# Kernel tuning notes

Hardware: AMD Instinct MI355X
Metric: run time of the kernel (lower is better)

Reference implementation:

```python
import jax, jax.numpy as jnp
import numpy as np


def spmm(src, dst, w, x, n):
    # out[i] = sum_{e: dst[e]==i} w[e] * x[src[e]]  == th.spmm(adj, x) with adj COO (dst=row, src=col)
    return jax.ops.segment_sum(x[src] * w[:, None], dst, num_segments=n)


def gcn(x, ei, w, W1, b1, W2, b2):
    # GCN.forward: relu(gc1(x, adj)) -> dropout(eval: identity) -> gc2(x, adj)
    n = x.shape[0]
    src, dst = ei[1], ei[0]
    h = jax.nn.relu(spmm(src, dst, w, x @ W1, n) + b1)
    return spmm(src, dst, w, h @ W2, n) + b2


def setup_inputs() -> dict:
    key = jax.random.key(0)
    ks = jax.random.split(key, 24)
    Nd, Ns = 100000, 50000
    Fd, Fs, H1, H2 = 256, 256, 256, 128
    DEG = 32
    Ed, Es = Nd * DEG, Ns * DEG
    inp = {}
    inp['drug_sim_feat'] = jax.random.normal(ks[0], (Nd, Fd), jnp.float32)
    inp['drug_edge_index'] = jax.random.randint(ks[1], (2, Ed), 0, Nd, jnp.int32)
    inp['drug_edge_weight'] = jax.random.uniform(ks[2], (Ed,), jnp.float32) / DEG
    inp['drug_feat_edge_index'] = jax.random.randint(ks[3], (2, Ed), 0, Nd, jnp.int32)
    inp['drug_feat_edge_weight'] = jax.random.uniform(ks[4], (Ed,), jnp.float32) / DEG
    inp['disease_sim_feat'] = jax.random.normal(ks[5], (Ns, Fs), jnp.float32)
    inp['dis_edge_index'] = jax.random.randint(ks[6], (2, Es), 0, Ns, jnp.int32)
    inp['dis_edge_weight'] = jax.random.uniform(ks[7], (Es,), jnp.float32) / DEG
    inp['dis_feat_edge_index'] = jax.random.randint(ks[8], (2, Es), 0, Ns, jnp.int32)
    inp['dis_feat_edge_weight'] = jax.random.uniform(ks[9], (Es,), jnp.float32) / DEG
    # params: uniform(-stdv, stdv), stdv = 1/sqrt(out_features) as in reset_parameters
    def unif(k, shape, out_f):
        s = 1.0 / np.sqrt(out_f)
        return jax.random.uniform(k, shape, jnp.float32, -s, s)
    inp['W1d'] = unif(ks[10], (Fd, H1), H1); inp['b1d'] = unif(ks[11], (H1,), H1)
    inp['W2d'] = unif(ks[12], (H1, H2), H2); inp['b2d'] = unif(ks[13], (H2,), H2)
    inp['W1s'] = unif(ks[14], (Fs, H1), H1); inp['b1s'] = unif(ks[15], (H1,), H1)
    inp['W2s'] = unif(ks[16], (H1, H2), H2); inp['b2s'] = unif(ks[17], (H2,), H2)
    # fusion Linears (nhid2*2 -> nhid2); kaiming-ish uniform
    fs = 1.0 / np.sqrt(2 * H2)
    inp['Wfd'] = jax.random.uniform(ks[18], (2 * H2, H2), jnp.float32, -fs, fs)
    inp['bfd'] = jax.random.uniform(ks[19], (H2,), jnp.float32, -fs, fs)
    inp['Wfs'] = jax.random.uniform(ks[20], (2 * H2, H2), jnp.float32, -fs, fs)
    inp['bfs'] = jax.random.uniform(ks[21], (H2,), jnp.float32, -fs, fs)
    return inp


def reference(drug_sim_feat, drug_edge_index, drug_edge_weight,
              drug_feat_edge_index, drug_feat_edge_weight,
              disease_sim_feat, dis_edge_index, dis_edge_weight,
              dis_feat_edge_index, dis_feat_edge_weight,
              W1d, b1d, W2d, b2d, W1s, b1s, W2s, b2s,
              Wfd, bfd, Wfs, bfs):
    # dropout in eval mode (identity)
    emb1_sim = gcn(drug_sim_feat, drug_edge_index, drug_edge_weight, W1d, b1d, W2d, b2d)
    emb2_sim = gcn(disease_sim_feat, dis_edge_index, dis_edge_weight, W1s, b1s, W2s, b2s)
    emb1_feat = gcn(drug_sim_feat, drug_feat_edge_index, drug_feat_edge_weight, W1d, b1d, W2d, b2d)
    emb2_feat = gcn(disease_sim_feat, dis_feat_edge_index, dis_feat_edge_weight, W1s, b1s, W2s, b2s)
    emb1 = jax.nn.relu(jnp.concatenate([emb1_sim, emb1_feat], axis=1) @ Wfd + bfd)
    emb2 = jax.nn.relu(jnp.concatenate([emb2_sim, emb2_feat], axis=1) @ Wfs + bfs)
    return (emb1, emb2, emb1_sim, emb1_feat, emb2_sim, emb2_feat)
```

## Files before the change

kernel.cpp:

```cpp
#include <hip/hip_runtime.h>

typedef _Float16 f16;
typedef __attribute__((ext_vector_type(8))) _Float16 f16x8;
typedef __attribute__((ext_vector_type(4))) float f32x4;

__device__ inline ushort f2h_bits(float f) {
    f16 h = (f16)f;
    return __builtin_bit_cast(ushort, h);
}

struct T6 {
    const float* s[6];
    ushort* d[6];
    int N[6];
};

__global__ __launch_bounds__(256) void transpose6_k(T6 a) {
    __shared__ ushort tile[32][33];
    const int z = blockIdx.z;
    const int K = 256, N = a.N[z];
    int k0 = blockIdx.x * 32, n0 = blockIdx.y * 32;
    if (n0 >= N) return;
    const float* W = a.s[z];
    ushort* Wt = a.d[z];
    int tx = threadIdx.x & 31, ty = threadIdx.x >> 5;
    #pragma unroll
    for (int i = 0; i < 32; i += 8)
        tile[ty + i][tx] = f2h_bits(W[(size_t)(k0 + ty + i) * N + n0 + tx]);
    __syncthreads();
    #pragma unroll
    for (int i = 0; i < 32; i += 8)
        Wt[(size_t)(n0 + ty + i) * K + k0 + tx] = tile[tx][ty + i];
}

struct GraphDesc {
    const int* ei;
    const float* w;
    int E, n, NB, bstoff;
    int* row_ptr;
    int2* perm;
};
struct G4 { GraphDesc g[4]; };

__global__ __launch_bounds__(256) void hist_b(G4 a, int* __restrict__ bcounts) {
    const GraphDesc& G = a.g[blockIdx.y];
    const int e0 = blockIdx.x * 4096;
    if (e0 >= G.E) return;
    __shared__ int h[512];
    int t = threadIdx.x;
    h[t] = 0; h[t + 256] = 0;
    __syncthreads();
    #pragma unroll
    for (int k = 0; k < 16; ++k) {
        int i = e0 + t + k * 256;
        if (i < G.E) atomicAdd(&h[((uint)G.ei[i]) >> 8], 1);
    }
    __syncthreads();
    int* bc = bcounts + blockIdx.y * 512;
    for (int b = t; b < 512; b += 256)
        if (h[b]) atomicAdd(&bc[b], h[b]);
}

__global__ __launch_bounds__(256) void scan_b(G4 a, const int* __restrict__ bcounts,
                                              int* __restrict__ bbase, int* __restrict__ bcursor) {
    const int gidx = blockIdx.x;
    const GraphDesc& G = a.g[gidx];
    const int* bc = bcounts + gidx * 512;
    int* base = bbase + gidx * 513;
    int* cur  = bcursor + gidx * 512;
    int t = threadIdx.x, lane = t & 63, wave = t >> 6;
    int v0 = bc[2 * t], v1 = bc[2 * t + 1];
    int s = v0 + v1;
    int incl = s;
    for (int off = 1; off < 64; off <<= 1) {
        int u = __shfl_up(incl, off);
        if (lane >= off) incl += u;
    }
    __shared__ int wsum[4];
    if (lane == 63) wsum[wave] = incl;
    __syncthreads();
    int excl = incl - s;
    for (int wv = 0; wv < wave; ++wv) excl += wsum[wv];
    base[2 * t] = excl;      cur[2 * t] = excl;
    base[2 * t + 1] = excl + v0; cur[2 * t + 1] = excl + v0;
    if (t == 0) { base[512] = G.E; G.row_ptr[G.n] = G.E; }
}

__global__ __launch_bounds__(256) void scatter_b(G4 a, int* __restrict__ bcursor,
                                                 int2* __restrict__ bst) {
    const GraphDesc& G = a.g[blockIdx.y];
    const int e0 = blockIdx.x * 4096;
    if (e0 >= G.E) return;
    __shared__ int hist[512], excl[512], sbase[512], lcur[512];
    __shared__ int2 stage[4096];
    __shared__ ushort sbin[4096];
    const int t = threadIdx.x, lane = t & 63, wave = t >> 6;
    const int cnt = min(4096, G.E - e0);
    int* bcur = bcursor + blockIdx.y * 512;

    hist[t] = 0; hist[t + 256] = 0;
    __syncthreads();

    int   d[16], s[16];
    float wv[16];
    #pragma unroll
    for (int k = 0; k < 16; ++k) {
        int i = t + k * 256;
        if (i < cnt) {
            d[k]  = G.ei[e0 + i];
            s[k]  = G.ei[(size_t)G.E + e0 + i];
            wv[k] = G.w[e0 + i];
            atomicAdd(&hist[((uint)d[k]) >> 8], 1);
        }
    }
    __syncthreads();

    {
        int v0 = hist[2 * t], v1 = hist[2 * t + 1];
        int sum = v0 + v1;
        int incl = sum;
        for (int off = 1; off < 64; off <<= 1) {
            int u = __shfl_up(incl, off);
            if (lane >= off) incl += u;
        }
        __shared__ int wsum[4];
        if (lane == 63) wsum[wave] = incl;
        __syncthreads();
        int e = incl - sum;
        for (int wvv = 0; wvv < wave; ++wvv) e += wsum[wvv];
        excl[2 * t] = e; excl[2 * t + 1] = e + v0;
    }
    __syncthreads();

    for (int b = t; b < 512; b += 256) {
        int c = hist[b];
        sbase[b] = c ? atomicAdd(&bcur[b], c) : 0;
        lcur[b] = excl[b];
    }
    __syncthreads();

    #pragma unroll
    for (int k = 0; k < 16; ++k) {
        int i = t + k * 256;
        if (i < cnt) {
            int bin = ((uint)d[k]) >> 8;
            int pos = atomicAdd(&lcur[bin], 1);
            stage[pos] = make_int2((s[k] << 8) | (d[k] & 255), __float_as_int(wv[k]));
            sbin[pos] = (ushort)bin;
        }
    }
    __syncthreads();

    #pragma unroll
    for (int k = 0; k < 16; ++k) {
        int i = t + k * 256;
        if (i < cnt) {
            int2 r = stage[i];
            int bin = sbin[i];
            bst[(size_t)G.bstoff + sbase[bin] + i - excl[bin]] = r;
        }
    }
}

__global__ __launch_bounds__(256) void finalize_b(G4 a, const int* __restrict__ bbase,
                                                  const int2* __restrict__ bst) {
    const GraphDesc& G = a.g[blockIdx.y];
    const int b = blockIdx.x;
    if (b >= G.NB) return;
    __shared__ int hist[256], cur[256], wsum[4];
    const int t = threadIdx.x, lane = t & 63, wave = t >> 6;
    const int* base = bbase + blockIdx.y * 513;
    const int lo = base[b], hi = base[b + 1];
    const int2* bg = bst + G.bstoff;
    hist[t] = 0;
    __syncthreads();
    for (int i = lo + t; i < hi; i += 256)
        atomicAdd(&hist[bg[i].x & 255], 1);
    __syncthreads();
    int v = hist[t];
    int incl = v;
    for (int off = 1; off < 64; off <<= 1) {
        int u = __shfl_up(incl, off);
        if (lane >= off) incl += u;
    }
    if (lane == 63) wsum[wave] = incl;
    __syncthreads();
    int excl = incl - v;
    for (int wv = 0; wv < wave; ++wv) excl += wsum[wv];
    const int r0 = b << 8;
    const int nrows = min(256, G.n - r0);
    if (t < nrows) G.row_ptr[r0 + t] = lo + excl;
    cur[t] = lo + excl;
    __syncthreads();
    for (int i = lo + t; i < hi; i += 256) {
        int2 r = bg[i];
        int local = r.x & 255;
        int slot = atomicAdd(&cur[local], 1);
        G.perm[slot] = make_int2(r.x >> 8, r.y);
    }
}

struct PairDesc {
    const int2* perm[2];
    const int*  rp[2];
    ushort*     outh[2];
};

template<int C>
__global__ __launch_bounds__(256) void spmm_pair_f16(
    const f16* __restrict__ x, PairDesc a, const float* __restrict__ bias, int n)
{
    const int g = blockIdx.y;
    const int wave = threadIdx.x >> 6, lane = threadIdx.x & 63;
    const int row = blockIdx.x * 4 + wave;
    if (row >= n) return;
    const int2* __restrict__ perm = a.perm[g];
    const int*  __restrict__ rp   = a.rp[g];
    const int F = 64 * C;
    const int e0 = rp[row], e1 = rp[row + 1];
    float acc[C] = {};
    const int laneoff = lane * C;

    for (int eb = e0; eb < e1; eb += 64) {
        int idx = eb + lane;
        int myS = 0; int myW = 0;
        if (idx < e1) { int2 rec = perm[idx]; myS = rec.x; myW = rec.y; }
        int m = min(64, e1 - eb);
        for (int j0 = 0; j0 < m; j0 += 8) {
            #pragma unroll
            for (int u = 0; u < 8; ++u) {
                int j = j0 + u;
                int   s = __builtin_amdgcn_readlane(myS, j);
                float w = __int_as_float(__builtin_amdgcn_readlane(myW, j));
                const f16* xr = x + (size_t)((uint)s * (uint)F) + laneoff;
                union { uint2 u2; f16 h[4]; } cv;
                cv.u2 = *reinterpret_cast<const uint2*>(xr);
                acc[0] = fmaf((float)cv.h[0], w, acc[0]);
                acc[1] = fmaf((float)cv.h[1], w, acc[1]);
                acc[2] = fmaf((float)cv.h[2], w, acc[2]);
                acc[3] = fmaf((float)cv.h[3], w, acc[3]);
            }
        }
    }

    #pragma unroll
    for (int c = 0; c < C; ++c) {
        float v = acc[c] + bias[laneoff + c];
        acc[c] = fmaxf(v, 0.f);
    }
    *reinterpret_cast<ushort4*>(a.outh[g] + (size_t)row * F + laneoff) =
        make_ushort4(f2h_bits(acc[0]), f2h_bits(acc[1]), f2h_bits(acc[2]), f2h_bits(acc[3]));
}

__global__ __launch_bounds__(256) void spmm_l2_f16(
    const f16* __restrict__ x,
    const int2* __restrict__ perm,
    const int* __restrict__ row_ptr, const float* __restrict__ bias,
    ushort* __restrict__ out_h, float* __restrict__ out_f, int n)
{
    const int wave = threadIdx.x >> 6, lane = threadIdx.x & 63;
    const int row = blockIdx.x * 4 + wave;
    if (row >= n) return;
    const int F = 128;
    const int e0 = row_ptr[row], e1 = row_ptr[row + 1];
    float acc[2] = {};
    const int laneoff = lane * 2;

    for (int eb = e0; eb < e1; eb += 64) {
        int idx = eb + lane;
        int myS = 0; int myW = 0;
        if (idx < e1) { int2 rec = perm[idx]; myS = rec.x; myW = rec.y; }
        int m = min(64, e1 - eb);
        for (int j0 = 0; j0 < m; j0 += 8) {
            #pragma unroll
            for (int u = 0; u < 8; ++u) {
                int j = j0 + u;
                int   s = __builtin_amdgcn_readlane(myS, j);
                float w = __int_as_float(__builtin_amdgcn_readlane(myW, j));
                union { uint u1; f16 h[2]; } cv;
                cv.u1 = *reinterpret_cast<const uint*>(x + (size_t)((uint)s * (uint)F) + laneoff);
                acc[0] = fmaf((float)cv.h[0], w, acc[0]);
                acc[1] = fmaf((float)cv.h[1], w, acc[1]);
            }
        }
    }

    acc[0] += bias[laneoff];
    acc[1] += bias[laneoff + 1];
    size_t ob = (size_t)row * F + laneoff;
    *reinterpret_cast<float2*>(out_f + ob) = make_float2(acc[0], acc[1]);
    *reinterpret_cast<ushort2*>(out_h + ob) = make_ushort2(f2h_bits(acc[0]), f2h_bits(acc[1]));
}

template<bool SWAP, bool CVTA, bool FUSE, bool RELU, bool BIAS, bool F32OUT>
__global__ __launch_bounds__(256) void gemm_mfma(
    const void* __restrict__ Av, const ushort* __restrict__ A2,
    const ushort* __restrict__ Bt, const float* __restrict__ bias,
    ushort* __restrict__ Ch, float* __restrict__ Cf,
    int M, int N, int K)
{
    __shared__ ushort Asb[128 * 32];
    __shared__ ushort Bsb[128 * 32];
    const int tid = threadIdx.x;
    const int lane = tid & 63, wave = tid >> 6;
    const int wr = wave >> 1, wc = wave & 1;
    const int bm = (SWAP ? blockIdx.y : blockIdx.x) * 128;
    const int bn = (SWAP ? blockIdx.x : blockIdx.y) * 128;

    f32x4 acc[4][4] = {};

    for (int k0 = 0; k0 < K; k0 += 32) {
        #pragma unroll
        for (int h = 0; h < 2; ++h) {
            int slot = tid + 256 * h;
            int r = slot >> 2, cb = slot & 3;
            int row = bm + r;
            uint4 v = make_uint4(0, 0, 0, 0);
            if (row < M) {
                int kk = k0 + cb * 8;
                if (CVTA) {
                    const float* Af = (const float*)Av;
                    float4 lo = *reinterpret_cast<const float4*>(Af + (size_t)row * K + kk);
                    float4 hi = *reinterpret_cast<const float4*>(Af + (size_t)row * K + kk + 4);
                    ushort h8[8] = { f2h_bits(lo.x), f2h_bits(lo.y), f2h_bits(lo.z), f2h_bits(lo.w),
                                     f2h_bits(hi.x), f2h_bits(hi.y), f2h_bits(hi.z), f2h_bits(hi.w) };
                    v = *reinterpret_cast<const uint4*>(h8);
                } else if (FUSE) {
                    const ushort* Ap = (kk < 128) ? (const ushort*)Av : A2;
                    v = *reinterpret_cast<const uint4*>(Ap + (size_t)row * 128 + (kk & 127));
                } else {
                    v = *reinterpret_cast<const uint4*>((const ushort*)Av + (size_t)row * K + kk);
                }
            }
            int scb = cb ^ ((r >> 1) & 3);
            *reinterpret_cast<uint4*>(&Asb[r * 32 + scb * 8]) = v;
        }
        #pragma unroll
        for (int h = 0; h < 2; ++h) {
            int slot = tid + 256 * h;
            int r = slot >> 2, cb = slot & 3;
            uint4 v = *reinterpret_cast<const uint4*>(Bt + (size_t)(bn + r) * K + k0 + cb * 8);
            int scb = cb ^ ((r >> 1) & 3);
            *reinterpret_cast<uint4*>(&Bsb[r * 32 + scb * 8]) = v;
        }
        __syncthreads();

        f16x8 fa[4], fb[4];
        #pragma unroll
        for (int i = 0; i < 4; ++i) {
            int r = wr * 64 + i * 16 + (lane & 15);
            int scb = (lane >> 4) ^ ((r >> 1) & 3);
            fa[i] = *reinterpret_cast<const f16x8*>(&Asb[r * 32 + scb * 8]);
        }
        #pragma unroll
        for (int j = 0; j < 4; ++j) {
            int r = wc * 64 + j * 16 + (lane & 15);
            int scb = (lane >> 4) ^ ((r >> 1) & 3);
            fb[j] = *reinterpret_cast<const f16x8*>(&Bsb[r * 32 + scb * 8]);
        }
        #pragma unroll
        for (int i = 0; i < 4; ++i)
            #pragma unroll
            for (int j = 0; j < 4; ++j)
                acc[i][j] = __builtin_amdgcn_mfma_f32_16x16x32_f16(fa[i], fb[j], acc[i][j], 0, 0, 0);
        __syncthreads();
    }

    #pragma unroll
    for (int i = 0; i < 4; ++i) {
        #pragma unroll
        for (int r4 = 0; r4 < 4; ++r4) {
            int row = bm + wr * 64 + i * 16 + (lane >> 4) * 4 + r4;
            if (row >= M) continue;
            #pragma unroll
            for (int j = 0; j < 4; ++j) {
                int col = bn + wc * 64 + j * 16 + (lane & 15);
                float v = acc[i][j][r4];
                if (BIAS) v += bias[col];
                if (RELU) v = fmaxf(v, 0.f);
                if (F32OUT) Cf[(size_t)row * N + col] = v;
                else        Ch[(size_t)row * N + col] = f2h_bits(v);
            }
        }
    }
}

extern "C" void kernel_launch(void* const* d_in, const int* in_sizes, int n_in,
                              void* d_out, int out_size, void* d_ws, size_t ws_size,
                              hipStream_t stream) {
    const float* Xd       = (const float*)d_in[0];
    const int*   eid_sim  = (const int*)  d_in[1];
    const float* wd_sim   = (const float*)d_in[2];
    const int*   eid_feat = (const int*)  d_in[3];
    const float* wd_feat  = (const float*)d_in[4];
    const float* Xs       = (const float*)d_in[5];
    const int*   eis_sim  = (const int*)  d_in[6];
    const float* ws_sim   = (const float*)d_in[7];
    const int*   eis_feat = (const int*)  d_in[8];
    const float* ws_feat  = (const float*)d_in[9];
    const float* W1d = (const float*)d_in[10]; const float* b1d = (const float*)d_in[11];
    const float* W2d = (const float*)d_in[12]; const float* b2d = (const float*)d_in[13];
    const float* W1s = (const float*)d_in[14]; const float* b1s = (const float*)d_in[15];
    const float* W2s = (const float*)d_in[16]; const float* b2s = (const float*)d_in[17];
    const float* Wfd = (const float*)d_in[18]; const float* bfd = (const float*)d_in[19];
    const float* Wfs = (const float*)d_in[20]; const float* bfs = (const float*)d_in[21];

    const int Fd = 256, H1 = 256, H2 = 128;
    const int Nd = in_sizes[0] / Fd;
    const int Ns = in_sizes[5] / Fd;
    const int Ed = in_sizes[2];
    const int Es = in_sizes[7];

    float* out    = (float*)d_out;
    float* o_emb1 = out;
    float* o_emb2 = o_emb1 + (size_t)Nd * H2;
    float* o_e1s  = o_emb2 + (size_t)Ns * H2;
    float* o_e1f  = o_e1s  + (size_t)Nd * H2;
    float* o_e2s  = o_e1f  + (size_t)Nd * H2;
    float* o_e2f  = o_e2s  + (size_t)Ns * H2;

    char* p = (char*)d_ws;
    auto alloc = [&](size_t bytes) { char* q = p; p += (bytes + 255) & ~(size_t)255; return q; };
    ushort* xw1   = (ushort*)alloc((size_t)Nd * 256 * 2);
    ushort* hbuf0 = (ushort*)alloc((size_t)Nd * 256 * 2);
    ushort* hbuf1 = (ushort*)alloc((size_t)Nd * 256 * 2);
    ushort* tbuf0 = (ushort*)alloc((size_t)Nd * 128 * 2);
    ushort* tbuf1 = (ushort*)alloc((size_t)Nd * 128 * 2);
    ushort* W1dt  = (ushort*)alloc(256 * 256 * 2);
    ushort* W2dt  = (ushort*)alloc(256 * 128 * 2);
    ushort* Wfdt  = (ushort*)alloc(256 * 128 * 2);
    ushort* W1st  = (ushort*)alloc(256 * 256 * 2);
    ushort* W2st  = (ushort*)alloc(256 * 128 * 2);
    ushort* Wfst  = (ushort*)alloc(256 * 128 * 2);
    int2*   perm0 = (int2*)alloc((size_t)Ed * 8);
    int2*   perm1 = (int2*)alloc((size_t)Ed * 8);
    int2*   perm2 = (int2*)alloc((size_t)Es * 8);
    int2*   perm3 = (int2*)alloc((size_t)Es * 8);
    int*    rp0   = (int*) alloc((size_t)(Nd + 1) * 4);
    int*    rp1   = (int*) alloc((size_t)(Nd + 1) * 4);
    int*    rp2   = (int*) alloc((size_t)(Ns + 1) * 4);
    int*    rp3   = (int*) alloc((size_t)(Ns + 1) * 4);
    int*    bcounts = (int*)alloc(4 * 512 * 4);
    int*    bbase   = (int*)alloc(4 * 513 * 4);
    int*    bcursor = (int*)alloc(4 * 512 * 4);
    int2*   bst  = (int2*)hbuf0;
    ushort* es_h = xw1;
    ushort* ef_h = xw1 + (size_t)Nd * 128;

    {
        T6 a;
        a.s[0] = W1d; a.s[1] = W2d; a.s[2] = Wfd; a.s[3] = W1s; a.s[4] = W2s; a.s[5] = Wfs;
        a.d[0] = W1dt; a.d[1] = W2dt; a.d[2] = Wfdt; a.d[3] = W1st; a.d[4] = W2st; a.d[5] = Wfst;
        a.N[0] = 256; a.N[1] = 128; a.N[2] = 128; a.N[3] = 256; a.N[4] = 128; a.N[5] = 128;
        transpose6_k<<<dim3(8, 8, 6), 256, 0, stream>>>(a);
    }

    G4 a;
    a.g[0] = { eid_sim,  wd_sim,  Ed, Nd, (Nd + 255) >> 8, 0,           rp0, perm0 };
    a.g[1] = { eid_feat, wd_feat, Ed, Nd, (Nd + 255) >> 8, Ed,          rp1, perm1 };
    a.g[2] = { eis_sim,  ws_sim,  Es, Ns, (Ns + 255) >> 8, 2 * Ed,      rp2, perm2 };
    a.g[3] = { eis_feat, ws_feat, Es, Ns, (Ns + 255) >> 8, 2 * Ed + Es, rp3, perm3 };
    {
        const int maxEB = (Ed + 4095) / 4096;
        const int maxNB = (Nd + 255) >> 8;
        hipMemsetAsync(bcounts, 0, 4 * 512 * 4, stream);
        hist_b<<<dim3(maxEB, 4), 256, 0, stream>>>(a, bcounts);
        scan_b<<<4, 256, 0, stream>>>(a, bcounts, bbase, bcursor);
        scatter_b<<<dim3(maxEB, 4), 256, 0, stream>>>(a, bcursor, bst);
        finalize_b<<<dim3(maxNB, 4), 256, 0, stream>>>(a, bbase, bst);
    }

    auto branch = [&](const float* X, int n,
                      const int2* pA, const int* rpA,
                      const int2* pB, const int* rpB,
                      const ushort* W1t, const float* b1,
                      const ushort* W2t, const float* b2,
                      const ushort* Wft, const float* bfu,
                      float* o_sim, float* o_feat, float* o_emb) {
        const int Mb = (n + 127) / 128;
        gemm_mfma<true, true, false, false, false, false><<<dim3(2, Mb), 256, 0, stream>>>(
            X, nullptr, W1t, nullptr, xw1, nullptr, n, 256, 256);
        PairDesc pd;
        pd.perm[0] = pA; pd.perm[1] = pB;
        pd.rp[0] = rpA;  pd.rp[1] = rpB;
        pd.outh[0] = hbuf0; pd.outh[1] = hbuf1;
        spmm_pair_f16<4><<<dim3((n + 3) / 4, 2), 256, 0, stream>>>(
            (const f16*)xw1, pd, b1, n);
        gemm_mfma<false, false, false, false, false, false><<<dim3(Mb, 1), 256, 0, stream>>>(
            hbuf0, nullptr, W2t, nullptr, tbuf0, nullptr, n, 128, 256);
        gemm_mfma<false, false, false, false, false, false><<<dim3(Mb, 1), 256, 0, stream>>>(
            hbuf1, nullptr, W2t, nullptr, tbuf1, nullptr, n, 128, 256);
        spmm_l2_f16<<<(n + 3) / 4, 256, 0, stream>>>(
            (const f16*)tbuf0, pA, rpA, b2, es_h, o_sim, n);
        spmm_l2_f16<<<(n + 3) / 4, 256, 0, stream>>>(
            (const f16*)tbuf1, pB, rpB, b2, ef_h, o_feat, n);
        gemm_mfma<false, false, true, true, true, true><<<dim3(Mb, 1), 256, 0, stream>>>(
            es_h, ef_h, Wft, bfu, nullptr, o_emb, n, 128, 256);
    };

    branch(Xd, Nd, perm0, rp0, perm1, rp1,
           W1dt, b1d, W2dt, b2d, Wfdt, bfd, o_e1s, o_e1f, o_emb1);
    branch(Xs, Ns, perm2, rp2, perm3, rp3,
           W1st, b1s, W2st, b2s, Wfst, bfs, o_e2s, o_e2f, o_emb2);
}
```

Baseline: 1.379 ms.

## Co-schedule drug and disease branch stages in fused heterogeneous kernels

Gives the disease branch its own workspace buffers so both GCN branches can proceed independently. Each fused launch combines one branch's GEMM blocks with the other branch's SpMM blocks, so the compute-bound MFMA work overlaps the memory-bound gather work. It also merges the two layer-2 SpMM launches into one grid. The cost is extra workspace, a sequential fallback when the workspace is too small, and a fat kernel whose register and LDS use is sized for the GEMM path, which may lower SpMM occupancy.

```diff
diff --git a/kernel.cpp b/kernel.cpp
--- a/kernel.cpp
+++ b/kernel.cpp
@@ -200,26 +200,37 @@
     }
 }
 
-struct PairDesc {
+struct PairA {
+    const f16* x;
     const int2* perm[2];
-    const int*  rp[2];
-    ushort*     outh[2];
+    const int* rp[2];
+    ushort* outh[2];
+    const float* bias;
+    int n, gx;
 };
 
-template<int C>
-__global__ __launch_bounds__(256) void spmm_pair_f16(
-    const f16* __restrict__ x, PairDesc a, const float* __restrict__ bias, int n)
-{
-    const int g = blockIdx.y;
+struct L2A {
+    const f16* x[2];
+    const int2* perm[2];
+    const int* rp[2];
+    ushort* outh[2];
+    float* outf[2];
+    const float* bias;
+    int n, gx;
+};
+
+__device__ __forceinline__ void spmm_pair_body(const PairA& a, int sb) {
+    const int g = sb / a.gx;
+    const int rb = sb % a.gx;
     const int wave = threadIdx.x >> 6, lane = threadIdx.x & 63;
-    const int row = blockIdx.x * 4 + wave;
-    if (row >= n) return;
+    const int row = rb * 4 + wave;
+    if (row >= a.n) return;
     const int2* __restrict__ perm = a.perm[g];
     const int*  __restrict__ rp   = a.rp[g];
-    const int F = 64 * C;
+    const int F = 256;
     const int e0 = rp[row], e1 = rp[row + 1];
-    float acc[C] = {};
-    const int laneoff = lane * C;
+    float acc[4] = {};
+    const int laneoff = lane * 4;
 
     for (int eb = e0; eb < e1; eb += 64) {
         int idx = eb + lane;
@@ -232,7 +243,7 @@
                 int j = j0 + u;
                 int   s = __builtin_amdgcn_readlane(myS, j);
                 float w = __int_as_float(__builtin_amdgcn_readlane(myW, j));
-                const f16* xr = x + (size_t)((uint)s * (uint)F) + laneoff;
+                const f16* xr = a.x + (size_t)((uint)s * (uint)F) + laneoff;
                 union { uint2 u2; f16 h[4]; } cv;
                 cv.u2 = *reinterpret_cast<const uint2*>(xr);
                 acc[0] = fmaf((float)cv.h[0], w, acc[0]);
@@ -244,25 +255,23 @@
     }
 
     #pragma unroll
-    for (int c = 0; c < C; ++c) {
-        float v = acc[c] + bias[laneoff + c];
-        acc[c] = fmaxf(v, 0.f);
-    }
+    for (int c = 0; c < 4; ++c)
+        acc[c] = fmaxf(acc[c] + a.bias[laneoff + c], 0.f);
     *reinterpret_cast<ushort4*>(a.outh[g] + (size_t)row * F + laneoff) =
         make_ushort4(f2h_bits(acc[0]), f2h_bits(acc[1]), f2h_bits(acc[2]), f2h_bits(acc[3]));
 }
 
-__global__ __launch_bounds__(256) void spmm_l2_f16(
-    const f16* __restrict__ x,
-    const int2* __restrict__ perm,
-    const int* __restrict__ row_ptr, const float* __restrict__ bias,
-    ushort* __restrict__ out_h, float* __restrict__ out_f, int n)
-{
+__device__ __forceinline__ void spmm_l2_body(const L2A& a, int sb) {
+    const int g = sb / a.gx;
+    const int rb = sb % a.gx;
     const int wave = threadIdx.x >> 6, lane = threadIdx.x & 63;
-    const int row = blockIdx.x * 4 + wave;
-    if (row >= n) return;
+    const int row = rb * 4 + wave;
+    if (row >= a.n) return;
+    const f16*  __restrict__ x    = a.x[g];
+    const int2* __restrict__ perm = a.perm[g];
+    const int*  __restrict__ rp   = a.rp[g];
     const int F = 128;
-    const int e0 = row_ptr[row], e1 = row_ptr[row + 1];
+    const int e0 = rp[row], e1 = rp[row + 1];
     float acc[2] = {};
     const int laneoff = lane * 2;
 
@@ -285,27 +294,32 @@
         }
     }
 
-    acc[0] += bias[laneoff];
-    acc[1] += bias[laneoff + 1];
+    acc[0] += a.bias[laneoff];
+    acc[1] += a.bias[laneoff + 1];
     size_t ob = (size_t)row * F + laneoff;
-    *reinterpret_cast<float2*>(out_f + ob) = make_float2(acc[0], acc[1]);
-    *reinterpret_cast<ushort2*>(out_h + ob) = make_ushort2(f2h_bits(acc[0]), f2h_bits(acc[1]));
-}
-
-template<bool SWAP, bool CVTA, bool FUSE, bool RELU, bool BIAS, bool F32OUT>
-__global__ __launch_bounds__(256) void gemm_mfma(
-    const void* __restrict__ Av, const ushort* __restrict__ A2,
-    const ushort* __restrict__ Bt, const float* __restrict__ bias,
-    ushort* __restrict__ Ch, float* __restrict__ Cf,
-    int M, int N, int K)
-{
+    *reinterpret_cast<float2*>(a.outf[g] + ob) = make_float2(acc[0], acc[1]);
+    *reinterpret_cast<ushort2*>(a.outh[g] + ob) = make_ushort2(f2h_bits(acc[0]), f2h_bits(acc[1]));
+}
+
+struct GemmJob {
+    const void* A;
+    const ushort* A2;
+    const ushort* Bt;
+    const float* bias;
+    ushort* Ch;
+    float* Cf;
+    int M, N, K, Nb;
+};
+
+template<bool CVTA, bool FUSE, bool RELU, bool BIAS, bool F32OUT>
+__device__ __forceinline__ void gemm_body(const GemmJob& j, int bm128, int bn128) {
     __shared__ ushort Asb[128 * 32];
     __shared__ ushort Bsb[128 * 32];
     const int tid = threadIdx.x;
     const int lane = tid & 63, wave = tid >> 6;
     const int wr = wave >> 1, wc = wave & 1;
-    const int bm = (SWAP ? blockIdx.y : blockIdx.x) * 128;
-    const int bn = (SWAP ? blockIdx.x : blockIdx.y) * 128;
+    const int bm = bm128 * 128, bn = bn128 * 128;
+    const int M = j.M, N = j.N, K = j.K;
 
     f32x4 acc[4][4] = {};
 
@@ -319,17 +333,17 @@
             if (row < M) {
                 int kk = k0 + cb * 8;
                 if (CVTA) {
-                    const float* Af = (const float*)Av;
+                    const float* Af = (const float*)j.A;
                     float4 lo = *reinterpret_cast<const float4*>(Af + (size_t)row * K + kk);
                     float4 hi = *reinterpret_cast<const float4*>(Af + (size_t)row * K + kk + 4);
                     ushort h8[8] = { f2h_bits(lo.x), f2h_bits(lo.y), f2h_bits(lo.z), f2h_bits(lo.w),
                                      f2h_bits(hi.x), f2h_bits(hi.y), f2h_bits(hi.z), f2h_bits(hi.w) };
                     v = *reinterpret_cast<const uint4*>(h8);
                 } else if (FUSE) {
-                    const ushort* Ap = (kk < 128) ? (const ushort*)Av : A2;
+                    const ushort* Ap = (kk < 128) ? (const ushort*)j.A : j.A2;
                     v = *reinterpret_cast<const uint4*>(Ap + (size_t)row * 128 + (kk & 127));
                 } else {
-                    v = *reinterpret_cast<const uint4*>((const ushort*)Av + (size_t)row * K + kk);
+                    v = *reinterpret_cast<const uint4*>((const ushort*)j.A + (size_t)row * K + kk);
                 }
             }
             int scb = cb ^ ((r >> 1) & 3);
@@ -339,7 +353,7 @@
         for (int h = 0; h < 2; ++h) {
             int slot = tid + 256 * h;
             int r = slot >> 2, cb = slot & 3;
-            uint4 v = *reinterpret_cast<const uint4*>(Bt + (size_t)(bn + r) * K + k0 + cb * 8);
+            uint4 v = *reinterpret_cast<const uint4*>(j.Bt + (size_t)(bn + r) * K + k0 + cb * 8);
             int scb = cb ^ ((r >> 1) & 3);
             *reinterpret_cast<uint4*>(&Bsb[r * 32 + scb * 8]) = v;
         }
@@ -353,16 +367,16 @@
             fa[i] = *reinterpret_cast<const f16x8*>(&Asb[r * 32 + scb * 8]);
         }
         #pragma unroll
-        for (int j = 0; j < 4; ++j) {
-            int r = wc * 64 + j * 16 + (lane & 15);
+        for (int jj = 0; jj < 4; ++jj) {
+            int r = wc * 64 + jj * 16 + (lane & 15);
             int scb = (lane >> 4) ^ ((r >> 1) & 3);
-            fb[j] = *reinterpret_cast<const f16x8*>(&Bsb[r * 32 + scb * 8]);
+            fb[jj] = *reinterpret_cast<const f16x8*>(&Bsb[r * 32 + scb * 8]);
         }
         #pragma unroll
         for (int i = 0; i < 4; ++i)
             #pragma unroll
-            for (int j = 0; j < 4; ++j)
-                acc[i][j] = __builtin_amdgcn_mfma_f32_16x16x32_f16(fa[i], fb[j], acc[i][j], 0, 0, 0);
+            for (int jj = 0; jj < 4; ++jj)
+                acc[i][jj] = __builtin_amdgcn_mfma_f32_16x16x32_f16(fa[i], fb[jj], acc[i][jj], 0, 0, 0);
         __syncthreads();
     }
 
@@ -373,15 +387,52 @@
             int row = bm + wr * 64 + i * 16 + (lane >> 4) * 4 + r4;
             if (row >= M) continue;
             #pragma unroll
-            for (int j = 0; j < 4; ++j) {
-                int col = bn + wc * 64 + j * 16 + (lane & 15);
-                float v = acc[i][j][r4];
-                if (BIAS) v += bias[col];
+            for (int jj = 0; jj < 4; ++jj) {
+                int col = bn + wc * 64 + jj * 16 + (lane & 15);
+                float v = acc[i][jj][r4];
+                if (BIAS) v += j.bias[col];
                 if (RELU) v = fmaxf(v, 0.f);
-                if (F32OUT) Cf[(size_t)row * N + col] = v;
-                else        Ch[(size_t)row * N + col] = f2h_bits(v);
+                if (F32OUT) j.Cf[(size_t)row * N + col] = v;
+                else        j.Ch[(size_t)row * N + col] = f2h_bits(v);
             }
         }
+    }
+}
+
+template<bool CVTA, bool FUSE, bool RELU, bool BIAS, bool F32OUT>
+__global__ __launch_bounds__(256) void gemm_k(GemmJob j) {
+    int bx = blockIdx.x;
+    gemm_body<CVTA, FUSE, RELU, BIAS, F32OUT>(j, bx / j.Nb, bx % j.Nb);
+}
+
+__global__ __launch_bounds__(256) void spmm_pair_k(PairA a) {
+    spmm_pair_body(a, blockIdx.x);
+}
+
+__global__ __launch_bounds__(256) void spmm_l2_k(L2A a) {
+    spmm_l2_body(a, blockIdx.x);
+}
+
+struct FatA {
+    PairA pa;
+    L2A la;
+    int spmm_blocks;
+    GemmJob j0, j1;
+    int jb0, jb1;
+};
+
+template<int SM, int GM>
+__global__ __launch_bounds__(256, 4) void fat_k(FatA a) {
+    int bx = blockIdx.x;
+    int gtot = a.jb0 + a.jb1;
+    if (bx < gtot) {
+        const GemmJob& j = (bx < a.jb0) ? a.j0 : a.j1;
+        int gb = (bx < a.jb0) ? bx : bx - a.jb0;
+        gemm_body<(GM == 0), (GM == 2), (GM == 2), (GM == 2), (GM == 2)>(j, gb / j.Nb, gb % j.Nb);
+    } else {
+        int sb = bx - gtot;
+        if (SM == 0) spmm_pair_body(a.pa, sb);
+        else         spmm_l2_body(a.la, sb);
     }
 }
 
@@ -405,7 +456,7 @@
     const float* Wfd = (const float*)d_in[18]; const float* bfd = (const float*)d_in[19];
     const float* Wfs = (const float*)d_in[20]; const float* bfs = (const float*)d_in[21];
 
-    const int Fd = 256, H1 = 256, H2 = 128;
+    const int Fd = 256, H2 = 128;
     const int Nd = in_sizes[0] / Fd;
     const int Ns = in_sizes[5] / Fd;
     const int Ed = in_sizes[2];
@@ -421,11 +472,7 @@
 
     char* p = (char*)d_ws;
     auto alloc = [&](size_t bytes) { char* q = p; p += (bytes + 255) & ~(size_t)255; return q; };
-    ushort* xw1   = (ushort*)alloc((size_t)Nd * 256 * 2);
-    ushort* hbuf0 = (ushort*)alloc((size_t)Nd * 256 * 2);
-    ushort* hbuf1 = (ushort*)alloc((size_t)Nd * 256 * 2);
-    ushort* tbuf0 = (ushort*)alloc((size_t)Nd * 128 * 2);
-    ushort* tbuf1 = (ushort*)alloc((size_t)Nd * 128 * 2);
+
     ushort* W1dt  = (ushort*)alloc(256 * 256 * 2);
     ushort* W2dt  = (ushort*)alloc(256 * 128 * 2);
     ushort* Wfdt  = (ushort*)alloc(256 * 128 * 2);
@@ -443,9 +490,24 @@
     int*    bcounts = (int*)alloc(4 * 512 * 4);
     int*    bbase   = (int*)alloc(4 * 513 * 4);
     int*    bcursor = (int*)alloc(4 * 512 * 4);
-    int2*   bst  = (int2*)hbuf0;
-    ushort* es_h = xw1;
-    ushort* ef_h = xw1 + (size_t)Nd * 128;
+    ushort* xw1d  = (ushort*)alloc((size_t)Nd * 256 * 2);
+    ushort* hbuf0 = (ushort*)alloc((size_t)Nd * 256 * 2);
+    ushort* hbuf1 = (ushort*)alloc((size_t)Nd * 256 * 2);
+    ushort* tbuf0 = (ushort*)alloc((size_t)Nd * 128 * 2);
+    ushort* tbuf1 = (ushort*)alloc((size_t)Nd * 128 * 2);
+    size_t seq_need = (size_t)(p - (char*)d_ws);
+    ushort* xw1s   = (ushort*)alloc((size_t)Ns * 256 * 2);
+    ushort* hbuf0s = (ushort*)alloc((size_t)Ns * 256 * 2);
+    ushort* hbuf1s = (ushort*)alloc((size_t)Ns * 256 * 2);
+    ushort* tbuf0s = (ushort*)alloc((size_t)Ns * 128 * 2);
+    ushort* tbuf1s = (ushort*)alloc((size_t)Ns * 128 * 2);
+    size_t ovl_need = (size_t)(p - (char*)d_ws);
+    const bool OVL = (ovl_need <= ws_size);
+
+    int2* bst = (int2*)hbuf0;
+
+    const int Mb_d = (Nd + 127) / 128, Mb_s = (Ns + 127) / 128;
+    const int gx_d = (Nd + 3) / 4,     gx_s = (Ns + 3) / 4;
 
     {
         T6 a;
@@ -470,36 +532,108 @@
         finalize_b<<<dim3(maxNB, 4), 256, 0, stream>>>(a, bbase, bst);
     }
 
-    auto branch = [&](const float* X, int n,
-                      const int2* pA, const int* rpA,
-                      const int2* pB, const int* rpB,
-                      const ushort* W1t, const float* b1,
-                      const ushort* W2t, const float* b2,
-                      const ushort* Wft, const float* bfu,
-                      float* o_sim, float* o_feat, float* o_emb) {
-        const int Mb = (n + 127) / 128;
-        gemm_mfma<true, true, false, false, false, false><<<dim3(2, Mb), 256, 0, stream>>>(
-            X, nullptr, W1t, nullptr, xw1, nullptr, n, 256, 256);
-        PairDesc pd;
-        pd.perm[0] = pA; pd.perm[1] = pB;
-        pd.rp[0] = rpA;  pd.rp[1] = rpB;
-        pd.outh[0] = hbuf0; pd.outh[1] = hbuf1;
-        spmm_pair_f16<4><<<dim3((n + 3) / 4, 2), 256, 0, stream>>>(
-            (const f16*)xw1, pd, b1, n);
-        gemm_mfma<false, false, false, false, false, false><<<dim3(Mb, 1), 256, 0, stream>>>(
-            hbuf0, nullptr, W2t, nullptr, tbuf0, nullptr, n, 128, 256);
-        gemm_mfma<false, false, false, false, false, false><<<dim3(Mb, 1), 256, 0, stream>>>(
-            hbuf1, nullptr, W2t, nullptr, tbuf1, nullptr, n, 128, 256);
-        spmm_l2_f16<<<(n + 3) / 4, 256, 0, stream>>>(
-            (const f16*)tbuf0, pA, rpA, b2, es_h, o_sim, n);
-        spmm_l2_f16<<<(n + 3) / 4, 256, 0, stream>>>(
-            (const f16*)tbuf1, pB, rpB, b2, ef_h, o_feat, n);
-        gemm_mfma<false, false, true, true, true, true><<<dim3(Mb, 1), 256, 0, stream>>>(
-            es_h, ef_h, Wft, bfu, nullptr, o_emb, n, 128, 256);
+    auto mkjob = [](const void* A, const ushort* A2, const ushort* Bt, const float* bias,
+                    ushort* Ch, float* Cf, int M, int N, int K) {
+        GemmJob j; j.A = A; j.A2 = A2; j.Bt = Bt; j.bias = bias;
+        j.Ch = Ch; j.Cf = Cf; j.M = M; j.N = N; j.K = K; j.Nb = N / 128; return j;
     };
 
-    branch(Xd, Nd, perm0, rp0, perm1, rp1,
-           W1dt, b1d, W2dt, b2d, Wfdt, bfd, o_e1s, o_e1f, o_emb1);
-    branch(Xs, Ns, perm2, rp2, perm3, rp3,
-           W1st, b1s, W2st, b2s, Wfst, bfs, o_e2s, o_e2f, o_emb2);
-}
+    if (OVL) {
+        ushort* es_d = xw1d;  ushort* ef_d = xw1d + (size_t)Nd * 128;
+        ushort* es_s = xw1s;  ushort* ef_s = xw1s + (size_t)Ns * 128;
+
+        gemm_k<true, false, false, false, false><<<2 * Mb_d, 256, 0, stream>>>(
+            mkjob(Xd, nullptr, W1dt, nullptr, xw1d, nullptr, Nd, 256, 256));
+
+        FatA f;
+        f = FatA{};
+        f.pa.x = (const f16*)xw1d;
+        f.pa.perm[0] = perm0; f.pa.perm[1] = perm1;
+        f.pa.rp[0] = rp0; f.pa.rp[1] = rp1;
+        f.pa.outh[0] = hbuf0; f.pa.outh[1] = hbuf1;
+        f.pa.bias = b1d; f.pa.n = Nd; f.pa.gx = gx_d;
+        f.spmm_blocks = 2 * gx_d;
+        f.j0 = mkjob(Xs, nullptr, W1st, nullptr, xw1s, nullptr, Ns, 256, 256);
+        f.jb0 = 2 * Mb_s; f.jb1 = 0; f.j1 = f.j0;
+        fat_k<0, 0><<<f.jb0 + f.spmm_blocks, 256, 0, stream>>>(f);
+
+        f = FatA{};
+        f.pa.x = (const f16*)xw1s;
+        f.pa.perm[0] = perm2; f.pa.perm[1] = perm3;
+        f.pa.rp[0] = rp2; f.pa.rp[1] = rp3;
+        f.pa.outh[0] = hbuf0s; f.pa.outh[1] = hbuf1s;
+        f.pa.bias = b1s; f.pa.n = Ns; f.pa.gx = gx_s;
+        f.spmm_blocks = 2 * gx_s;
+        f.j0 = mkjob(hbuf0, nullptr, W2dt, nullptr, tbuf0, nullptr, Nd, 128, 256);
+        f.j1 = mkjob(hbuf1, nullptr, W2dt, nullptr, tbuf1, nullptr, Nd, 128, 256);
+        f.jb0 = Mb_d; f.jb1 = Mb_d;
+        fat_k<0, 1><<<f.jb0 + f.jb1 + f.spmm_blocks, 256, 0, stream>>>(f);
+
+        f = FatA{};
+        f.la.x[0] = (const f16*)tbuf0; f.la.x[1] = (const f16*)tbuf1;
+        f.la.perm[0] = perm0; f.la.perm[1] = perm1;
+        f.la.rp[0] = rp0; f.la.rp[1] = rp1;
+        f.la.outh[0] = es_d; f.la.outh[1] = ef_d;
+        f.la.outf[0] = o_e1s; f.la.outf[1] = o_e1f;
+        f.la.bias = b2d; f.la.n = Nd; f.la.gx = gx_d;
+        f.spmm_blocks = 2 * gx_d;
+        f.j0 = mkjob(hbuf0s, nullptr, W2st, nullptr, tbuf0s, nullptr, Ns, 128, 256);
+        f.j1 = mkjob(hbuf1s, nullptr, W2st, nullptr, tbuf1s, nullptr, Ns, 128, 256);
+        f.jb0 = Mb_s; f.jb1 = Mb_s;
+        fat_k<1, 1><<<f.jb0 + f.jb1 + f.spmm_blocks, 256, 0, stream>>>(f);
+
+        f = FatA{};
+        f.la.x[0] = (const f16*)tbuf0s; f.la.x[1] = (const f16*)tbuf1s;
+        f.la.perm[0] = perm2; f.la.perm[1] = perm3;
+        f.la.rp[0] = rp2; f.la.rp[1] = rp3;
+        f.la.outh[0] = es_s; f.la.outh[1] = ef_s;
+        f.la.outf[0] = o_e2s; f.la.outf[1] = o_e2f;
+        f.la.bias = b2s; f.la.n = Ns; f.la.gx = gx_s;
+        f.spmm_blocks = 2 * gx_s;
+        f.j0 = mkjob(es_d, ef_d, Wfdt, bfd, nullptr, o_emb1, Nd, 128, 256);
+        f.jb0 = Mb_d; f.jb1 = 0; f.j1 = f.j0;
+        fat_k<1, 2><<<f.jb0 + f.spmm_blocks, 256, 0, stream>>>(f);
+
+        gemm_k<false, true, true, true, true><<<Mb_s, 256, 0, stream>>>(
+            mkjob(es_s, ef_s, Wfst, bfs, nullptr, o_emb2, Ns, 128, 256));
+    } else {
+        auto branch = [&](const float* X, int n, int gx, int Mb,
+                          const int2* pA, const int* rpA,
+                          const int2* pB, const int* rpB,
+                          const ushort* W1t, const float* b1,
+                          const ushort* W2t, const float* b2,
+                          const ushort* Wft, const float* bfu,
+                          float* o_sim, float* o_feat, float* o_emb) {
+            ushort* es_h = xw1d;
+            ushort* ef_h = xw1d + (size_t)n * 128;
+            gemm_k<true, false, false, false, false><<<2 * Mb, 256, 0, stream>>>(
+                mkjob(X, nullptr, W1t, nullptr, xw1d, nullptr, n, 256, 256));
+            PairA pa;
+            pa.x = (const f16*)xw1d;
+            pa.perm[0] = pA; pa.perm[1] = pB;
+            pa.rp[0] = rpA;  pa.rp[1] = rpB;
+            pa.outh[0] = hbuf0; pa.outh[1] = hbuf1;
+            pa.bias = b1; pa.n = n; pa.gx = gx;
+            spmm_pair_k<<<2 * gx, 256, 0, stream>>>(pa);
+            gemm_k<false, false, false, false, false><<<Mb, 256, 0, stream>>>(
+                mkjob(hbuf0, nullptr, W2t, nullptr, tbuf0, nullptr, n, 128, 256));
+            gemm_k<false, false, false, false, false><<<Mb, 256, 0, stream>>>(
+                mkjob(hbuf1, nullptr, W2t, nullptr, tbuf1, nullptr, n, 128, 256));
+            L2A la;
+            la.x[0] = (const f16*)tbuf0; la.x[1] = (const f16*)tbuf1;
+            la.perm[0] = pA; la.perm[1] = pB;
+            la.rp[0] = rpA;  la.rp[1] = rpB;
+            la.outh[0] = es_h; la.outh[1] = ef_h;
+            la.outf[0] = o_sim; la.outf[1] = o_feat;
+            la.bias = b2; la.n = n; la.gx = gx;
+            spmm_l2_k<<<2 * gx, 256, 0, stream>>>(la);
+            gemm_k<false, true, true, true, true><<<Mb, 256, 0, stream>>>(
+                mkjob(es_h, ef_h, Wft, bfu, nullptr, o_emb, n, 128, 256));
+        };
+        branch(Xd, Nd, gx_d, Mb_d, perm0, rp0, perm1, rp1,
+               W1dt, b1d, W2dt, b2d, Wfdt, bfd, o_e1s, o_e1f, o_emb1);
+        branch(Xs, Ns, gx_s, Mb_s, perm2, rp2, perm3, rp3,
+               W1st, b1s, W2st, b2s, Wfst, bfs, o_e2s, o_e2f, o_emb2);
+    }
+    (void)seq_need;
+}
```

Result: no change. 1.400 ms (+1.5%).
